# Performance work log

Hardware: AMD Instinct MI355X
Metric: run time of the kernel (lower is better)

## Reference

```python
import jax, jax.numpy as jnp
import numpy as np

N, E, EP, D = 50000, 600000, 200000, 128
L = 3  # gnn layers


def _w(k, shape):
    # Kaiming-ish init: scale by 1/sqrt(fan_in)
    return jax.random.normal(k, shape, jnp.float32) / jnp.sqrt(jnp.float32(shape[-2]))


def setup_inputs() -> dict:
    key = jax.random.key(0)
    ks = jax.random.split(key, 20)
    x = jax.random.normal(ks[0], (N, D), jnp.float32)
    edge_attr = jax.random.normal(ks[1], (E, 1), jnp.float32)
    edge_index = jax.random.randint(ks[2], (2, E), 0, N, jnp.int64)
    predict_edge_index = jax.random.randint(ks[3], (2, EP), 0, N, jnp.int64)
    return {
        "x": x,
        "edge_attr": edge_attr,
        "edge_index": edge_index,
        "predict_edge_index": predict_edge_index,
        # SAGEConv params per layer: out = lin_l(mean_aggr) + lin_r(x); lin_r has no bias
        "Wl": _w(ks[4], (L, D, D)),
        "bl": jnp.zeros((L, D), jnp.float32),
        "Wr": _w(ks[5], (L, D, D)),
        # edge update MLPs: layer0 in=2D+1, layers 1..L-1 in=3D
        "euW0": _w(ks[6], (2 * D + 1, D)),
        "euB0": jnp.zeros((D,), jnp.float32),
        "euW": _w(ks[7], (L - 1, 3 * D, D)),
        "euB": jnp.zeros((L - 1, D), jnp.float32),
        # node post MLP
        "pW1": _w(ks[8], (D, D)), "pb1": jnp.zeros((D,), jnp.float32),
        "pW2": _w(ks[9], (D, D)), "pb2": jnp.zeros((D,), jnp.float32),
        # edge predict MLP (predict_mode=0: concat of two node embeddings)
        "qW1": _w(ks[10], (2 * D, D)), "qb1": jnp.zeros((D,), jnp.float32),
        "qW2": _w(ks[11], (D, 1)), "qb2": jnp.zeros((1,), jnp.float32),
    }


def reference(x, edge_attr, edge_index, predict_edge_index,
              Wl, bl, Wr, euW0, euB0, euW, euB,
              pW1, pb1, pW2, pb2, qW1, qb1, qW2, qb2):
    # dropout p=0.0 / eval mode -> identity
    src, dst = edge_index[0], edge_index[1]
    n = x.shape[0]
    deg = jax.ops.segment_sum(jnp.ones(src.shape, jnp.float32), dst, num_segments=n)
    deg = jnp.maximum(deg, 1.0)[:, None]
    for l in range(L):
        # SAGEConv: mean-aggregate source features at destinations
        aggr = jax.ops.segment_sum(x[src], dst, num_segments=n) / deg
        x = jax.nn.relu(aggr @ Wl[l] + bl[l] + x @ Wr[l])
        # edge update: gather endpoints, concat with edge_attr, Linear+ReLU (+outer relu no-op)
        cat = jnp.concatenate([x[src], x[dst], edge_attr], axis=-1)
        if l == 0:
            edge_attr = jax.nn.relu(cat @ euW0 + euB0)
        else:
            edge_attr = jax.nn.relu(cat @ euW[l - 1] + euB[l - 1])
    # node post MLP
    x = jax.nn.relu(x @ pW1 + pb1) @ pW2 + pb2
    # predict_mode=0: gather pair endpoints and score
    xi = x[predict_edge_index[0]]
    xj = x[predict_edge_index[1]]
    h = jnp.concatenate([xi, xj], axis=-1)
    y = jax.nn.relu(h @ qW1 + qb1) @ qW2 + qb2  # [EP, 1]
    return y
```

## Files before the change

### kernel.cpp

```cpp
#include <hip/hip_runtime.h>


typedef __attribute__((ext_vector_type(8))) short bf16x8;
typedef __attribute__((ext_vector_type(4))) float f32x4;

__device__ __forceinline__ unsigned short f2bf(float x) {
  unsigned u = __float_as_uint(x);
  u += 0x7fffu + ((u >> 16) & 1u);
  return (unsigned short)(u >> 16);
}
__device__ __forceinline__ float bf2f(unsigned short h) {
  return __uint_as_float(((unsigned)h) << 16);
}
__device__ __forceinline__ float lo16f(unsigned u) { return __uint_as_float(u << 16); }
__device__ __forceinline__ float hi16f(unsigned u) { return __uint_as_float(u & 0xffff0000u); }

__device__ __forceinline__ void gload_lds16(const void* g, void* l) {
  __builtin_amdgcn_global_load_lds(
      (const __attribute__((address_space(1))) unsigned int*)g,
      (__attribute__((address_space(3))) unsigned int*)l, 16, 0, 0);
}

__global__ void k_count(const int* __restrict__ dst, int* __restrict__ cnt, int E) {
  int i = blockIdx.x * blockDim.x + threadIdx.x;
  if (i < E) atomicAdd(&cnt[dst[i]], 1);
}

__global__ void k_scan1(const int* __restrict__ cnt, int* __restrict__ rs,
                        float* __restrict__ degf, int* __restrict__ bsum, int n) {
  __shared__ int wsum[16];
  __shared__ int wpre[16];
  const int tid = threadIdx.x;
  const int lane = tid & 63;
  const int wv = tid >> 6;
  int i = blockIdx.x * 1024 + tid;
  int v = (i < n) ? cnt[i] : 0;
  int s = v;
#pragma unroll
  for (int off = 1; off < 64; off <<= 1) {
    int t = __shfl_up(s, off);
    if (lane >= off) s += t;
  }
  if (lane == 63) wsum[wv] = s;
  __syncthreads();
  if (tid < 16) {
    int t = wsum[tid];
    int ss = t;
#pragma unroll
    for (int off = 1; off < 16; off <<= 1) {
      int u = __shfl_up(ss, off);
      if (tid >= off) ss += u;
    }
    wpre[tid] = ss - t;
  }
  __syncthreads();
  if (i < n) {
    rs[i] = s - v + wpre[wv];
    degf[i] = (float)(v > 0 ? v : 1);
  }
  if (tid == 1023) bsum[blockIdx.x] = wpre[15] + wsum[15];
}

__global__ void k_scan3(int* __restrict__ rs, const int* __restrict__ bsum,
                        int* __restrict__ cursor, int n, int nb) {
  __shared__ int boff_s[64];
  __shared__ int total_s;
  int tid = threadIdx.x;
  if (tid < 64) {
    int v = (tid < nb) ? bsum[tid] : 0;
    int s = v;
#pragma unroll
    for (int off = 1; off < 64; off <<= 1) {
      int t = __shfl_up(s, off);
      if (tid >= off) s += t;
    }
    boff_s[tid] = s - v;
    if (tid == 63) total_s = s;
  }
  __syncthreads();
  int i = blockIdx.x * blockDim.x + tid;
  if (i < n) {
    int r = rs[i] + boff_s[i >> 10];
    rs[i] = r;
    cursor[i] = r;
  }
  if (blockIdx.x == 0 && tid == 0) rs[n] = total_s;
}

__global__ void k_scatter(const int* __restrict__ src, const int* __restrict__ dst,
                          int* __restrict__ cursor, int* __restrict__ csr, int E) {
  int i = blockIdx.x * blockDim.x + threadIdx.x;
  if (i < E) {
    int p = atomicAdd(&cursor[dst[i]], 1);
    csr[p] = src[i];
  }
}

__global__ void k_split(const float* __restrict__ x, unsigned* __restrict__ X,
                        long n2) {
  long g = (long)blockIdx.x * blockDim.x + threadIdx.x;
  if (g >= n2) return;
  float2 v = ((const float2*)x)[g];
  unsigned short hx = f2bf(v.x), hy = f2bf(v.y);
  unsigned short lx = f2bf(v.x - bf2f(hx)), ly = f2bf(v.y - bf2f(hy));
  long row = g >> 6, p = g & 63;
  X[row * 128 + p] = (unsigned)hx | ((unsigned)hy << 16);
  X[row * 128 + 64 + p] = (unsigned)lx | ((unsigned)ly << 16);
}

__global__ void k_packAll(const float* __restrict__ Wl, const float* __restrict__ Wr,
                          const float* __restrict__ pW1, const float* __restrict__ pW2,
                          const float* __restrict__ qW1,
                          unsigned short* __restrict__ hi,
                          unsigned short* __restrict__ lo) {
  int gid = blockIdx.x * blockDim.x + threadIdx.x;
  if (gid >= 10 * 2048) return;
  int mat = gid >> 11;
  const float* Wm;
  if (mat < 3) Wm = Wl + (size_t)mat * 16384;
  else if (mat < 6) Wm = Wr + (size_t)(mat - 3) * 16384;
  else if (mat == 6) Wm = pW1;
  else if (mat == 7) Wm = pW2;
  else Wm = qW1 + (size_t)(mat - 8) * 16384;
  int lane = gid & 63;
  int f = (gid >> 6) & 31;
  int nt = f >> 2, ks = f & 3;
  int nn = nt * 16 + (lane & 15);
  int k0 = ks * 32 + 8 * (lane >> 4);
  size_t dst = (size_t)gid * 8;
#pragma unroll
  for (int r = 0; r < 8; ++r) {
    float w = Wm[(size_t)(k0 + r) * 128 + nn];
    unsigned short h = f2bf(w);
    hi[dst + r] = h;
    lo[dst + r] = f2bf(w - bf2f(h));
  }
}

__global__ void k_biasuv(const float* __restrict__ qb1, float* __restrict__ b) {
  int i = threadIdx.x;
  b[i] = (i < 128) ? qb1[i] : 0.f;
}

__global__ void k_aggr(const unsigned short* __restrict__ X,
                       const int* __restrict__ csr, const int* __restrict__ rs,
                       const float* __restrict__ degf,
                       unsigned short* __restrict__ Bd, int n) {
  int gid = blockIdx.x * blockDim.x + threadIdx.x;
  int wid = gid >> 6, lane = gid & 63;
  if (wid >= n) return;
  int s = rs[wid], e = rs[wid + 1];
  const int h = lane >> 4;
  const int o16 = (lane & 15) * 8;
  float a0 = 0.f, a1 = 0.f, a2 = 0.f, a3 = 0.f;
  float a4 = 0.f, a5 = 0.f, a6 = 0.f, a7 = 0.f;
  int j = s;
  for (; j + 7 < e; j += 8) {
    int n0 = csr[j + h];
    int n1 = csr[j + 4 + h];
    uint4 v0 = *(const uint4*)(X + (size_t)n0 * 256 + o16);
    uint4 v1 = *(const uint4*)(X + (size_t)n1 * 256 + o16);
    a0 += lo16f(v0.x) + lo16f(v1.x);
    a1 += hi16f(v0.x) + hi16f(v1.x);
    a2 += lo16f(v0.y) + lo16f(v1.y);
    a3 += hi16f(v0.y) + hi16f(v1.y);
    a4 += lo16f(v0.z) + lo16f(v1.z);
    a5 += hi16f(v0.z) + hi16f(v1.z);
    a6 += lo16f(v0.w) + lo16f(v1.w);
    a7 += hi16f(v0.w) + hi16f(v1.w);
  }
  for (; j < e; j += 4) {
    int idx = j + h;
    bool ok = idx < e;
    int nn = ok ? csr[idx] : 0;
    uint4 v = *(const uint4*)(X + (size_t)nn * 256 + o16);
    float m = ok ? 1.f : 0.f;
    a0 += m * lo16f(v.x); a1 += m * hi16f(v.x);
    a2 += m * lo16f(v.y); a3 += m * hi16f(v.y);
    a4 += m * lo16f(v.z); a5 += m * hi16f(v.z);
    a6 += m * lo16f(v.w); a7 += m * hi16f(v.w);
  }
  a0 += __shfl_xor(a0, 16); a1 += __shfl_xor(a1, 16);
  a2 += __shfl_xor(a2, 16); a3 += __shfl_xor(a3, 16);
  a4 += __shfl_xor(a4, 16); a5 += __shfl_xor(a5, 16);
  a6 += __shfl_xor(a6, 16); a7 += __shfl_xor(a7, 16);
  a0 += __shfl_xor(a0, 32); a1 += __shfl_xor(a1, 32);
  a2 += __shfl_xor(a2, 32); a3 += __shfl_xor(a3, 32);
  a4 += __shfl_xor(a4, 32); a5 += __shfl_xor(a5, 32);
  a6 += __shfl_xor(a6, 32); a7 += __shfl_xor(a7, 32);
  if (lane < 16) {
    float inv = 1.0f / degf[wid];
    unsigned short h0 = f2bf(a0 * inv), h1 = f2bf(a1 * inv);
    unsigned short h2 = f2bf(a2 * inv), h3 = f2bf(a3 * inv);
    unsigned short h4 = f2bf(a4 * inv), h5 = f2bf(a5 * inv);
    unsigned short h6 = f2bf(a6 * inv), h7 = f2bf(a7 * inv);
    uint4 oh;
    oh.x = (unsigned)h0 | ((unsigned)h1 << 16);
    oh.y = (unsigned)h2 | ((unsigned)h3 << 16);
    oh.z = (unsigned)h4 | ((unsigned)h5 << 16);
    oh.w = (unsigned)h6 | ((unsigned)h7 << 16);
    *(uint4*)(Bd + (size_t)wid * 128 + o16) = oh;
  }
}

template <int NPHASE, int EPI, int A0DENSE>
__global__ __launch_bounds__(512, 4) void k_gemm(
    const unsigned short* __restrict__ A0, const unsigned short* __restrict__ A1,
    const unsigned short* __restrict__ W0h, const unsigned short* __restrict__ W0l,
    const unsigned short* __restrict__ W1h, const unsigned short* __restrict__ W1l,
    const float* __restrict__ bias, unsigned short* __restrict__ O, int nrows,
    long uvW, long uvO) {
  __shared__ unsigned short smem[8 * 4096];
  unsigned short* smh = smem;
  unsigned short* sml = smem + 8 * 2048;

  const long yb = blockIdx.y;
  W0h += yb * uvW;
  W0l += yb * uvW;
  bias += yb * 128;
  O += yb * uvO;

  const int tid = threadIdx.x;
  const int lane = tid & 63;
  const int wv = tid >> 6;
  const long row0 = ((long)blockIdx.x * 8 + wv) * 16;
  const bool active = row0 < nrows;
  const int kgrp = (lane >> 4) * 8;

  long r = row0 + (lane & 15);
  const long arow = (r < nrows) ? r : (long)(nrows - 1);

#pragma unroll
  for (int k = 0; k < 4; ++k) {
    int t = tid + k * 512;
    gload_lds16((const uint4*)W0h + t, (uint4*)smh + t);
    gload_lds16((const uint4*)W0l + t, (uint4*)sml + t);
  }

  bf16x8 a0h[4], a0l[4], a1h[4], a1l[4];
  if (active) {
#pragma unroll
    for (int ks = 0; ks < 4; ++ks) {
      if (A0DENSE) {
        a0h[ks] = *(const bf16x8*)(A0 + arow * 128 + ks * 32 + kgrp);
      } else {
        a0h[ks] = *(const bf16x8*)(A0 + arow * 256 + ks * 32 + kgrp);
        a0l[ks] = *(const bf16x8*)(A0 + arow * 256 + 128 + ks * 32 + kgrp);
      }
      if (NPHASE == 2) {
        a1h[ks] = *(const bf16x8*)(A1 + arow * 256 + ks * 32 + kgrp);
        a1l[ks] = *(const bf16x8*)(A1 + arow * 256 + 128 + ks * 32 + kgrp);
      }
    }
  }

  f32x4 zero = {0.f, 0.f, 0.f, 0.f};
  f32x4 acc[8];
#pragma unroll
  for (int t = 0; t < 8; ++t) acc[t] = zero;

  __syncthreads();

  if (active) {
#pragma unroll
    for (int ks = 0; ks < 4; ++ks) {
#pragma unroll
      for (int nt = 0; nt < 8; ++nt) {
        const bf16x8 b_h = *(const bf16x8*)(smh + (nt * 4 + ks) * 512 + lane * 8);
        const bf16x8 b_l = *(const bf16x8*)(sml + (nt * 4 + ks) * 512 + lane * 8);
        acc[nt] = __builtin_amdgcn_mfma_f32_16x16x32_bf16(b_h, a0h[ks], acc[nt], 0, 0, 0);
        if (!A0DENSE)
          acc[nt] = __builtin_amdgcn_mfma_f32_16x16x32_bf16(b_h, a0l[ks], acc[nt], 0, 0, 0);
        acc[nt] = __builtin_amdgcn_mfma_f32_16x16x32_bf16(b_l, a0h[ks], acc[nt], 0, 0, 0);
      }
    }
  }

  if (NPHASE == 2) {
    __syncthreads();
#pragma unroll
    for (int k = 0; k < 4; ++k) {
      int t = tid + k * 512;
      gload_lds16((const uint4*)W1h + t, (uint4*)smh + t);
      gload_lds16((const uint4*)W1l + t, (uint4*)sml + t);
    }
    __syncthreads();
    if (active) {
#pragma unroll
      for (int ks = 0; ks < 4; ++ks) {
#pragma unroll
        for (int nt = 0; nt < 8; ++nt) {
          const bf16x8 b_h = *(const bf16x8*)(smh + (nt * 4 + ks) * 512 + lane * 8);
          const bf16x8 b_l = *(const bf16x8*)(sml + (nt * 4 + ks) * 512 + lane * 8);
          acc[nt] = __builtin_amdgcn_mfma_f32_16x16x32_bf16(b_h, a1h[ks], acc[nt], 0, 0, 0);
          acc[nt] = __builtin_amdgcn_mfma_f32_16x16x32_bf16(b_h, a1l[ks], acc[nt], 0, 0, 0);
          acc[nt] = __builtin_amdgcn_mfma_f32_16x16x32_bf16(b_l, a1h[ks], acc[nt], 0, 0, 0);
        }
      }
    }
  }
  if (!active) return;

  const int cq = (lane >> 4) * 4;
  const long row = row0 + (lane & 15);
  if (row >= nrows) return;
#pragma unroll
  for (int nt = 0; nt < 8; ++nt) {
    const int col = nt * 16 + cq;
    float4 bv = *(const float4*)(bias + col);
    float v0 = acc[nt][0] + bv.x;
    float v1 = acc[nt][1] + bv.y;
    float v2 = acc[nt][2] + bv.z;
    float v3 = acc[nt][3] + bv.w;
    if (EPI == 0) {
      v0 = fmaxf(v0, 0.f); v1 = fmaxf(v1, 0.f);
      v2 = fmaxf(v2, 0.f); v3 = fmaxf(v3, 0.f);
    }
    unsigned short h0 = f2bf(v0), h1 = f2bf(v1), h2 = f2bf(v2), h3 = f2bf(v3);
    uint2 oh;
    oh.x = (unsigned)h0 | ((unsigned)h1 << 16);
    oh.y = (unsigned)h2 | ((unsigned)h3 << 16);
    if (EPI == 2) {
      *(uint2*)(O + row * 128 + col) = oh;
    } else {
      uint2 ol;
      ol.x = (unsigned)f2bf(v0 - bf2f(h0)) | ((unsigned)f2bf(v1 - bf2f(h1)) << 16);
      ol.y = (unsigned)f2bf(v2 - bf2f(h2)) | ((unsigned)f2bf(v3 - bf2f(h3)) << 16);
      *(uint2*)(O + row * 256 + col) = oh;
      *(uint2*)(O + row * 256 + 128 + col) = ol;
    }
  }
}

__global__ __launch_bounds__(256) void k_pair(
    const unsigned short* __restrict__ u, const unsigned short* __restrict__ v,
    const int* __restrict__ ps, const int* __restrict__ pd,
    const float* __restrict__ qW2, const float* __restrict__ qb2,
    float* __restrict__ out, int EP) {
  int gid = blockIdx.x * blockDim.x + threadIdx.x;
  long wid = gid >> 6;
  int lane = gid & 63;
  int sub = lane & 15, g = lane >> 4;
  long base = wid * 8;
  if (base >= EP) return;
  float4 q0 = *(const float4*)(qW2 + sub * 8);
  float4 q1 = *(const float4*)(qW2 + sub * 8 + 4);
  float qb = qb2[0];

  long p0 = base + g;
  long p1 = base + 4 + g;
  long c0 = (p0 < EP) ? p0 : (EP - 1);
  long c1 = (p1 < EP) ? p1 : (EP - 1);
  int i0 = ps[c0], j0 = pd[c0];
  int i1 = ps[c1], j1 = pd[c1];
  uint4 a0 = *(const uint4*)(u + (size_t)i0 * 128 + sub * 8);
  uint4 b0 = *(const uint4*)(v + (size_t)j0 * 128 + sub * 8);
  uint4 a1 = *(const uint4*)(u + (size_t)i1 * 128 + sub * 8);
  uint4 b1 = *(const uint4*)(v + (size_t)j1 * 128 + sub * 8);

  float s0, s1;
  {
    float t;
    t = fmaxf(lo16f(a0.x) + lo16f(b0.x), 0.f) * q0.x;
    t = fmaf(fmaxf(hi16f(a0.x) + hi16f(b0.x), 0.f), q0.y, t);
    t = fmaf(fmaxf(lo16f(a0.y) + lo16f(b0.y), 0.f), q0.z, t);
    t = fmaf(fmaxf(hi16f(a0.y) + hi16f(b0.y), 0.f), q0.w, t);
    t = fmaf(fmaxf(lo16f(a0.z) + lo16f(b0.z), 0.f), q1.x, t);
    t = fmaf(fmaxf(hi16f(a0.z) + hi16f(b0.z), 0.f), q1.y, t);
    t = fmaf(fmaxf(lo16f(a0.w) + lo16f(b0.w), 0.f), q1.z, t);
    t = fmaf(fmaxf(hi16f(a0.w) + hi16f(b0.w), 0.f), q1.w, t);
    s0 = t;
    t = fmaxf(lo16f(a1.x) + lo16f(b1.x), 0.f) * q0.x;
    t = fmaf(fmaxf(hi16f(a1.x) + hi16f(b1.x), 0.f), q0.y, t);
    t = fmaf(fmaxf(lo16f(a1.y) + lo16f(b1.y), 0.f), q0.z, t);
    t = fmaf(fmaxf(hi16f(a1.y) + hi16f(b1.y), 0.f), q0.w, t);
    t = fmaf(fmaxf(lo16f(a1.z) + lo16f(b1.z), 0.f), q1.x, t);
    t = fmaf(fmaxf(hi16f(a1.z) + hi16f(b1.z), 0.f), q1.y, t);
    t = fmaf(fmaxf(lo16f(a1.w) + lo16f(b1.w), 0.f), q1.z, t);
    t = fmaf(fmaxf(hi16f(a1.w) + hi16f(b1.w), 0.f), q1.w, t);
    s1 = t;
  }
#pragma unroll
  for (int m = 1; m < 16; m <<= 1) {
    s0 += __shfl_xor(s0, m);
    s1 += __shfl_xor(s1, m);
  }
  if (sub == 0) {
    if (p0 < EP) out[p0] = s0 + qb;
    if (p1 < EP) out[p1] = s1 + qb;
  }
}

extern "C" void kernel_launch(void* const* d_in, const int* in_sizes, int n_in,
                              void* d_out, int out_size, void* d_ws, size_t ws_size,
                              hipStream_t stream) {
  const float* x_in = (const float*)d_in[0];
  const int* ei = (const int*)d_in[2];
  const int* pe = (const int*)d_in[3];
  const float* Wl = (const float*)d_in[4];
  const float* bl = (const float*)d_in[5];
  const float* Wr = (const float*)d_in[6];
  const float* pW1 = (const float*)d_in[11];
  const float* pb1 = (const float*)d_in[12];
  const float* pW2 = (const float*)d_in[13];
  const float* pb2 = (const float*)d_in[14];
  const float* qW1 = (const float*)d_in[15];
  const float* qb1 = (const float*)d_in[16];
  const float* qW2 = (const float*)d_in[17];
  const float* qb2 = (const float*)d_in[18];

  const int N = in_sizes[0] / 128;
  const int E = in_sizes[2] / 2;
  const int EP = in_sizes[3] / 2;
  const int* e_src = ei;
  const int* e_dst = ei + E;
  const int* p_src = pe;
  const int* p_dst = pe + EP;

  char* ws = (char*)d_ws;
  size_t off = 0;
  auto alloc = [&](size_t bytes) {
    void* p = ws + off;
    off += (bytes + 511) & ~(size_t)511;
    return p;
  };
  unsigned short* X = (unsigned short*)alloc((size_t)N * 256 * 2);
  unsigned short* B = (unsigned short*)alloc((size_t)N * 256 * 2);
  int* deg_i = (int*)alloc((size_t)N * 4);
  int* rs = (int*)alloc((size_t)(N + 1) * 4);
  int* cursor = (int*)alloc((size_t)N * 4);
  float* degf = (float*)alloc((size_t)N * 4);
  int* csr = (int*)alloc((size_t)E * 4);
  int* bsum = (int*)alloc(64 * 4);
  unsigned short* Whi = (unsigned short*)alloc((size_t)10 * 16384 * 2);
  unsigned short* Wlo = (unsigned short*)alloc((size_t)10 * 16384 * 2);
  float* biasuv = (float*)alloc(256 * 4);

  const size_t MS = 16384;
  const int nb = (N + 1023) / 1024;

  hipMemsetAsync(deg_i, 0, (size_t)N * 4, stream);
  k_biasuv<<<1, 256, 0, stream>>>(qb1, biasuv);

  k_packAll<<<(10 * 2048 + 255) / 256, 256, 0, stream>>>(Wl, Wr, pW1, pW2, qW1,
                                                         Whi, Wlo);

  long n2 = (long)N * 64;
  k_split<<<(int)((n2 + 255) / 256), 256, 0, stream>>>(x_in, (unsigned*)X, n2);

  k_count<<<(E + 255) / 256, 256, 0, stream>>>(e_dst, deg_i, E);
  k_scan1<<<nb, 1024, 0, stream>>>(deg_i, rs, degf, bsum, N);
  k_scan3<<<(N + 255) / 256, 256, 0, stream>>>(rs, bsum, cursor, N, nb);
  k_scatter<<<(E + 255) / 256, 256, 0, stream>>>(e_src, e_dst, cursor, csr, E);

  const int gmm = (N + 127) / 128;
  const int agblocks = (N + 3) / 4;
  for (int l = 0; l < 3; ++l) {
    k_aggr<<<agblocks, 256, 0, stream>>>(X, csr, rs, degf, B, N);
    k_gemm<2, 0, 1><<<gmm, 512, 0, stream>>>(
        B, X, Whi + (size_t)l * MS, Wlo + (size_t)l * MS,
        Whi + (size_t)(3 + l) * MS, Wlo + (size_t)(3 + l) * MS,
        bl + (size_t)l * 128, X, N, 0, 0);
  }
  k_gemm<1, 0, 0><<<gmm, 512, 0, stream>>>(
      X, nullptr, Whi + 6 * MS, Wlo + 6 * MS, nullptr, nullptr, pb1, B, N, 0, 0);
  k_gemm<1, 1, 0><<<gmm, 512, 0, stream>>>(
      B, nullptr, Whi + 7 * MS, Wlo + 7 * MS, nullptr, nullptr, pb2, X, N, 0, 0);
  unsigned short* u = B;
  unsigned short* v = B + (size_t)N * 128;
  k_gemm<1, 2, 0><<<dim3(gmm, 2), 512, 0, stream>>>(
      X, nullptr, Whi + 8 * MS, Wlo + 8 * MS, nullptr, nullptr, biasuv, u, N,
      (long)MS, (long)N * 128);
  k_pair<<<(EP + 31) / 32, 256, 0, stream>>>(u, v, p_src, p_dst, qW2, qb2,
                                             (float*)d_out, EP);
}
```

Measured before the change: 314.8 us.

## Fuse post-MLP and pair-projection GEMMs into one kernel with LDS intermediates

The node post-MLP (two GEMMs) and the two halves of the qW1 projection were separate launches that each round-tripped hi/lo split activations through global memory. They now run in one kernel, k_post. Each wave keeps its 16-row tile in a swizzled LDS scratch between stages and reloads weights per stage. This removes three launches and the global writes and reads of the intermediates. In exchange it adds serialized weight reloads with block-wide barriers and lowers the occupancy hint to 2 blocks per CU.

```diff
diff --git a/kernel.cpp b/kernel.cpp
--- a/kernel.cpp
+++ b/kernel.cpp
@@ -135,11 +135,6 @@
     hi[dst + r] = h;
     lo[dst + r] = f2bf(w - bf2f(h));
   }
-}
-
-__global__ void k_biasuv(const float* __restrict__ qb1, float* __restrict__ b) {
-  int i = threadIdx.x;
-  b[i] = (i < 128) ? qb1[i] : 0.f;
 }
 
 __global__ void k_aggr(const unsigned short* __restrict__ X,
@@ -203,22 +198,65 @@
   }
 }
 
-template <int NPHASE, int EPI, int A0DENSE>
+__device__ __forceinline__ void mm3term(f32x4 acc[8], const bf16x8 a_h[4],
+                                        const bf16x8 a_l[4],
+                                        const unsigned short* smh,
+                                        const unsigned short* sml, int lane) {
+#pragma unroll
+  for (int ks = 0; ks < 4; ++ks)
+#pragma unroll
+    for (int nt = 0; nt < 8; ++nt) {
+      const bf16x8 b_h = *(const bf16x8*)(smh + (nt * 4 + ks) * 512 + lane * 8);
+      const bf16x8 b_l = *(const bf16x8*)(sml + (nt * 4 + ks) * 512 + lane * 8);
+      acc[nt] = __builtin_amdgcn_mfma_f32_16x16x32_bf16(b_h, a_h[ks], acc[nt], 0, 0, 0);
+      acc[nt] = __builtin_amdgcn_mfma_f32_16x16x32_bf16(b_h, a_l[ks], acc[nt], 0, 0, 0);
+      acc[nt] = __builtin_amdgcn_mfma_f32_16x16x32_bf16(b_l, a_h[ks], acc[nt], 0, 0, 0);
+    }
+}
+
+template <bool RELU>
+__device__ __forceinline__ void t_store(const f32x4 acc[8], const float* bias,
+                                        unsigned short* tw, int r16, int cq) {
+#pragma unroll
+  for (int nt = 0; nt < 8; ++nt) {
+    int col = nt * 16 + cq;
+    float4 bv = *(const float4*)(bias + col);
+    float v0 = acc[nt][0] + bv.x, v1 = acc[nt][1] + bv.y;
+    float v2 = acc[nt][2] + bv.z, v3 = acc[nt][3] + bv.w;
+    if (RELU) {
+      v0 = fmaxf(v0, 0.f); v1 = fmaxf(v1, 0.f);
+      v2 = fmaxf(v2, 0.f); v3 = fmaxf(v3, 0.f);
+    }
+    unsigned short h0 = f2bf(v0), h1 = f2bf(v1), h2 = f2bf(v2), h3 = f2bf(v3);
+    uint2 oh, ol;
+    oh.x = (unsigned)h0 | ((unsigned)h1 << 16);
+    oh.y = (unsigned)h2 | ((unsigned)h3 << 16);
+    ol.x = (unsigned)f2bf(v0 - bf2f(h0)) | ((unsigned)f2bf(v1 - bf2f(h1)) << 16);
+    ol.y = (unsigned)f2bf(v2 - bf2f(h2)) | ((unsigned)f2bf(v3 - bf2f(h3)) << 16);
+    int idx = (r16 * 128 + col) ^ ((r16 & 7) << 3);
+    *(uint2*)(tw + idx) = oh;
+    *(uint2*)(tw + 2048 + idx) = ol;
+  }
+}
+
+__device__ __forceinline__ void t_load(bf16x8 a_h[4], bf16x8 a_l[4],
+                                       const unsigned short* tw, int r16, int kgrp) {
+#pragma unroll
+  for (int ks = 0; ks < 4; ++ks) {
+    int idx = (r16 * 128 + ks * 32 + kgrp) ^ ((r16 & 7) << 3);
+    a_h[ks] = *(const bf16x8*)(tw + idx);
+    a_l[ks] = *(const bf16x8*)(tw + 2048 + idx);
+  }
+}
+
 __global__ __launch_bounds__(512, 4) void k_gemm(
     const unsigned short* __restrict__ A0, const unsigned short* __restrict__ A1,
     const unsigned short* __restrict__ W0h, const unsigned short* __restrict__ W0l,
     const unsigned short* __restrict__ W1h, const unsigned short* __restrict__ W1l,
-    const float* __restrict__ bias, unsigned short* __restrict__ O, int nrows,
-    long uvW, long uvO) {
-  __shared__ unsigned short smem[8 * 4096];
+    const float* __restrict__ bias, unsigned short* __restrict__ O, int nrows) {
+  __shared__ unsigned short smem[32768];
   unsigned short* smh = smem;
-  unsigned short* sml = smem + 8 * 2048;
-
-  const long yb = blockIdx.y;
-  W0h += yb * uvW;
-  W0l += yb * uvW;
-  bias += yb * 128;
-  O += yb * uvO;
+  unsigned short* sml = smem + 16384;
 
   const int tid = threadIdx.x;
   const int lane = tid & 63;
@@ -237,20 +275,13 @@
     gload_lds16((const uint4*)W0l + t, (uint4*)sml + t);
   }
 
-  bf16x8 a0h[4], a0l[4], a1h[4], a1l[4];
+  bf16x8 a0h[4], a1h[4], a1l[4];
   if (active) {
 #pragma unroll
     for (int ks = 0; ks < 4; ++ks) {
-      if (A0DENSE) {
-        a0h[ks] = *(const bf16x8*)(A0 + arow * 128 + ks * 32 + kgrp);
-      } else {
-        a0h[ks] = *(const bf16x8*)(A0 + arow * 256 + ks * 32 + kgrp);
-        a0l[ks] = *(const bf16x8*)(A0 + arow * 256 + 128 + ks * 32 + kgrp);
-      }
-      if (NPHASE == 2) {
-        a1h[ks] = *(const bf16x8*)(A1 + arow * 256 + ks * 32 + kgrp);
-        a1l[ks] = *(const bf16x8*)(A1 + arow * 256 + 128 + ks * 32 + kgrp);
-      }
+      a0h[ks] = *(const bf16x8*)(A0 + arow * 128 + ks * 32 + kgrp);
+      a1h[ks] = *(const bf16x8*)(A1 + arow * 256 + ks * 32 + kgrp);
+      a1l[ks] = *(const bf16x8*)(A1 + arow * 256 + 128 + ks * 32 + kgrp);
     }
   }
 
@@ -263,43 +294,27 @@
 
   if (active) {
 #pragma unroll
-    for (int ks = 0; ks < 4; ++ks) {
+    for (int ks = 0; ks < 4; ++ks)
 #pragma unroll
       for (int nt = 0; nt < 8; ++nt) {
         const bf16x8 b_h = *(const bf16x8*)(smh + (nt * 4 + ks) * 512 + lane * 8);
         const bf16x8 b_l = *(const bf16x8*)(sml + (nt * 4 + ks) * 512 + lane * 8);
         acc[nt] = __builtin_amdgcn_mfma_f32_16x16x32_bf16(b_h, a0h[ks], acc[nt], 0, 0, 0);
-        if (!A0DENSE)
-          acc[nt] = __builtin_amdgcn_mfma_f32_16x16x32_bf16(b_h, a0l[ks], acc[nt], 0, 0, 0);
         acc[nt] = __builtin_amdgcn_mfma_f32_16x16x32_bf16(b_l, a0h[ks], acc[nt], 0, 0, 0);
       }
-    }
-  }
-
-  if (NPHASE == 2) {
-    __syncthreads();
-#pragma unroll
-    for (int k = 0; k < 4; ++k) {
-      int t = tid + k * 512;
-      gload_lds16((const uint4*)W1h + t, (uint4*)smh + t);
-      gload_lds16((const uint4*)W1l + t, (uint4*)sml + t);
-    }
-    __syncthreads();
-    if (active) {
-#pragma unroll
-      for (int ks = 0; ks < 4; ++ks) {
-#pragma unroll
-        for (int nt = 0; nt < 8; ++nt) {
-          const bf16x8 b_h = *(const bf16x8*)(smh + (nt * 4 + ks) * 512 + lane * 8);
-          const bf16x8 b_l = *(const bf16x8*)(sml + (nt * 4 + ks) * 512 + lane * 8);
-          acc[nt] = __builtin_amdgcn_mfma_f32_16x16x32_bf16(b_h, a1h[ks], acc[nt], 0, 0, 0);
-          acc[nt] = __builtin_amdgcn_mfma_f32_16x16x32_bf16(b_h, a1l[ks], acc[nt], 0, 0, 0);
-          acc[nt] = __builtin_amdgcn_mfma_f32_16x16x32_bf16(b_l, a1h[ks], acc[nt], 0, 0, 0);
-        }
-      }
-    }
-  }
+  }
+
+  __syncthreads();
+#pragma unroll
+  for (int k = 0; k < 4; ++k) {
+    int t = tid + k * 512;
+    gload_lds16((const uint4*)W1h + t, (uint4*)smh + t);
+    gload_lds16((const uint4*)W1l + t, (uint4*)sml + t);
+  }
+  __syncthreads();
   if (!active) return;
+
+  mm3term(acc, a1h, a1l, smh, sml, lane);
 
   const int cq = (lane >> 4) * 4;
   const long row = row0 + (lane & 15);
@@ -308,27 +323,141 @@
   for (int nt = 0; nt < 8; ++nt) {
     const int col = nt * 16 + cq;
     float4 bv = *(const float4*)(bias + col);
-    float v0 = acc[nt][0] + bv.x;
-    float v1 = acc[nt][1] + bv.y;
-    float v2 = acc[nt][2] + bv.z;
-    float v3 = acc[nt][3] + bv.w;
-    if (EPI == 0) {
-      v0 = fmaxf(v0, 0.f); v1 = fmaxf(v1, 0.f);
-      v2 = fmaxf(v2, 0.f); v3 = fmaxf(v3, 0.f);
+    float v0 = fmaxf(acc[nt][0] + bv.x, 0.f);
+    float v1 = fmaxf(acc[nt][1] + bv.y, 0.f);
+    float v2 = fmaxf(acc[nt][2] + bv.z, 0.f);
+    float v3 = fmaxf(acc[nt][3] + bv.w, 0.f);
+    unsigned short h0 = f2bf(v0), h1 = f2bf(v1), h2 = f2bf(v2), h3 = f2bf(v3);
+    uint2 oh, ol;
+    oh.x = (unsigned)h0 | ((unsigned)h1 << 16);
+    oh.y = (unsigned)h2 | ((unsigned)h3 << 16);
+    ol.x = (unsigned)f2bf(v0 - bf2f(h0)) | ((unsigned)f2bf(v1 - bf2f(h1)) << 16);
+    ol.y = (unsigned)f2bf(v2 - bf2f(h2)) | ((unsigned)f2bf(v3 - bf2f(h3)) << 16);
+    *(uint2*)(O + row * 256 + col) = oh;
+    *(uint2*)(O + row * 256 + 128 + col) = ol;
+  }
+}
+
+__global__ __launch_bounds__(512, 2) void k_post(
+    const unsigned short* __restrict__ X,
+    const unsigned short* __restrict__ W1h, const unsigned short* __restrict__ W1l,
+    const unsigned short* __restrict__ W2h, const unsigned short* __restrict__ W2l,
+    const unsigned short* __restrict__ W3h, const unsigned short* __restrict__ W3l,
+    const unsigned short* __restrict__ W4h, const unsigned short* __restrict__ W4l,
+    const float* __restrict__ b1, const float* __restrict__ b2,
+    const float* __restrict__ b3, const float* __restrict__ b4,
+    unsigned short* __restrict__ U, unsigned short* __restrict__ V, int nrows) {
+  __shared__ unsigned short smem[32768];
+  unsigned short* smh = smem;
+  unsigned short* sml = smem + 16384;
+
+  const int tid = threadIdx.x;
+  const int lane = tid & 63;
+  const int wv = tid >> 6;
+  const long row0 = ((long)blockIdx.x * 8 + wv) * 16;
+  const bool active = row0 < nrows;
+  const int kgrp = (lane >> 4) * 8;
+  const int r16 = lane & 15;
+  const int cq = (lane >> 4) * 4;
+  unsigned short* tw = smem + wv * 4096;
+
+  long rr = row0 + r16;
+  const long arow = (rr < nrows) ? rr : (long)(nrows - 1);
+  const long row = row0 + r16;
+
+#pragma unroll
+  for (int k = 0; k < 4; ++k) {
+    int t = tid + k * 512;
+    gload_lds16((const uint4*)W1h + t, (uint4*)smh + t);
+    gload_lds16((const uint4*)W1l + t, (uint4*)sml + t);
+  }
+  bf16x8 a_h[4], a_l[4];
+  if (active) {
+#pragma unroll
+    for (int ks = 0; ks < 4; ++ks) {
+      a_h[ks] = *(const bf16x8*)(X + arow * 256 + ks * 32 + kgrp);
+      a_l[ks] = *(const bf16x8*)(X + arow * 256 + 128 + ks * 32 + kgrp);
     }
-    unsigned short h0 = f2bf(v0), h1 = f2bf(v1), h2 = f2bf(v2), h3 = f2bf(v3);
+  }
+  f32x4 zero = {0.f, 0.f, 0.f, 0.f};
+  f32x4 acc[8];
+#pragma unroll
+  for (int t = 0; t < 8; ++t) acc[t] = zero;
+
+  __syncthreads();
+  if (active) mm3term(acc, a_h, a_l, smh, sml, lane);
+  __syncthreads();
+
+  if (active) {
+    t_store<true>(acc, b1, tw, r16, cq);
+    t_load(a_h, a_l, tw, r16, kgrp);
+  }
+  __syncthreads();
+
+#pragma unroll
+  for (int k = 0; k < 4; ++k) {
+    int t = tid + k * 512;
+    gload_lds16((const uint4*)W2h + t, (uint4*)smh + t);
+    gload_lds16((const uint4*)W2l + t, (uint4*)sml + t);
+  }
+#pragma unroll
+  for (int t = 0; t < 8; ++t) acc[t] = zero;
+  __syncthreads();
+  if (active) mm3term(acc, a_h, a_l, smh, sml, lane);
+  __syncthreads();
+
+  if (active) {
+    t_store<false>(acc, b2, tw, r16, cq);
+    t_load(a_h, a_l, tw, r16, kgrp);
+  }
+  __syncthreads();
+
+#pragma unroll
+  for (int k = 0; k < 4; ++k) {
+    int t = tid + k * 512;
+    gload_lds16((const uint4*)W3h + t, (uint4*)smh + t);
+    gload_lds16((const uint4*)W3l + t, (uint4*)sml + t);
+  }
+#pragma unroll
+  for (int t = 0; t < 8; ++t) acc[t] = zero;
+  __syncthreads();
+  if (active) mm3term(acc, a_h, a_l, smh, sml, lane);
+  if (active && row < nrows) {
+#pragma unroll
+    for (int nt = 0; nt < 8; ++nt) {
+      const int col = nt * 16 + cq;
+      float4 bv = *(const float4*)(b3 + col);
+      unsigned short h0 = f2bf(acc[nt][0] + bv.x), h1 = f2bf(acc[nt][1] + bv.y);
+      unsigned short h2 = f2bf(acc[nt][2] + bv.z), h3 = f2bf(acc[nt][3] + bv.w);
+      uint2 oh;
+      oh.x = (unsigned)h0 | ((unsigned)h1 << 16);
+      oh.y = (unsigned)h2 | ((unsigned)h3 << 16);
+      *(uint2*)(U + row * 128 + col) = oh;
+    }
+  }
+  __syncthreads();
+
+#pragma unroll
+  for (int k = 0; k < 4; ++k) {
+    int t = tid + k * 512;
+    gload_lds16((const uint4*)W4h + t, (uint4*)smh + t);
+    gload_lds16((const uint4*)W4l + t, (uint4*)sml + t);
+  }
+#pragma unroll
+  for (int t = 0; t < 8; ++t) acc[t] = zero;
+  __syncthreads();
+  if (!active || row >= nrows) return;
+  mm3term(acc, a_h, a_l, smh, sml, lane);
+#pragma unroll
+  for (int nt = 0; nt < 8; ++nt) {
+    const int col = nt * 16 + cq;
+    float4 bv = *(const float4*)(b4 + col);
+    unsigned short h0 = f2bf(acc[nt][0] + bv.x), h1 = f2bf(acc[nt][1] + bv.y);
+    unsigned short h2 = f2bf(acc[nt][2] + bv.z), h3 = f2bf(acc[nt][3] + bv.w);
     uint2 oh;
     oh.x = (unsigned)h0 | ((unsigned)h1 << 16);
     oh.y = (unsigned)h2 | ((unsigned)h3 << 16);
-    if (EPI == 2) {
-      *(uint2*)(O + row * 128 + col) = oh;
-    } else {
-      uint2 ol;
-      ol.x = (unsigned)f2bf(v0 - bf2f(h0)) | ((unsigned)f2bf(v1 - bf2f(h1)) << 16);
-      ol.y = (unsigned)f2bf(v2 - bf2f(h2)) | ((unsigned)f2bf(v3 - bf2f(h3)) << 16);
-      *(uint2*)(O + row * 256 + col) = oh;
-      *(uint2*)(O + row * 256 + 128 + col) = ol;
-    }
+    *(uint2*)(V + row * 128 + col) = oh;
   }
 }
 
@@ -434,13 +563,13 @@
   int* bsum = (int*)alloc(64 * 4);
   unsigned short* Whi = (unsigned short*)alloc((size_t)10 * 16384 * 2);
   unsigned short* Wlo = (unsigned short*)alloc((size_t)10 * 16384 * 2);
-  float* biasuv = (float*)alloc(256 * 4);
+  float* zerob = (float*)alloc(128 * 4);
 
   const size_t MS = 16384;
   const int nb = (N + 1023) / 1024;
 
   hipMemsetAsync(deg_i, 0, (size_t)N * 4, stream);
-  k_biasuv<<<1, 256, 0, stream>>>(qb1, biasuv);
+  hipMemsetAsync(zerob, 0, 128 * 4, stream);
 
   k_packAll<<<(10 * 2048 + 255) / 256, 256, 0, stream>>>(Wl, Wr, pW1, pW2, qW1,
                                                          Whi, Wlo);
@@ -457,20 +586,17 @@
   const int agblocks = (N + 3) / 4;
   for (int l = 0; l < 3; ++l) {
     k_aggr<<<agblocks, 256, 0, stream>>>(X, csr, rs, degf, B, N);
-    k_gemm<2, 0, 1><<<gmm, 512, 0, stream>>>(
+    k_gemm<<<gmm, 512, 0, stream>>>(
         B, X, Whi + (size_t)l * MS, Wlo + (size_t)l * MS,
         Whi + (size_t)(3 + l) * MS, Wlo + (size_t)(3 + l) * MS,
-        bl + (size_t)l * 128, X, N, 0, 0);
-  }
-  k_gemm<1, 0, 0><<<gmm, 512, 0, stream>>>(
-      X, nullptr, Whi + 6 * MS, Wlo + 6 * MS, nullptr, nullptr, pb1, B, N, 0, 0);
-  k_gemm<1, 1, 0><<<gmm, 512, 0, stream>>>(
-      B, nullptr, Whi + 7 * MS, Wlo + 7 * MS, nullptr, nullptr, pb2, X, N, 0, 0);
+        bl + (size_t)l * 128, X, N);
+  }
   unsigned short* u = B;
   unsigned short* v = B + (size_t)N * 128;
-  k_gemm<1, 2, 0><<<dim3(gmm, 2), 512, 0, stream>>>(
-      X, nullptr, Whi + 8 * MS, Wlo + 8 * MS, nullptr, nullptr, biasuv, u, N,
-      (long)MS, (long)N * 128);
+  k_post<<<gmm, 512, 0, stream>>>(
+      X, Whi + 6 * MS, Wlo + 6 * MS, Whi + 7 * MS, Wlo + 7 * MS,
+      Whi + 8 * MS, Wlo + 8 * MS, Whi + 9 * MS, Wlo + 9 * MS,
+      pb1, pb2, qb1, zerob, u, v, N);
   k_pair<<<(EP + 31) / 32, 256, 0, stream>>>(u, v, p_src, p_dst, qW2, qb2,
                                              (float*)d_out, EP);
 }
```

Result: faster. 287.9 us (-8.5%).
